# Kernel tuning notes

Measured on AMD Instinct MI355X. Metric: run time of the kernel, lower is better.

Reference implementation:

```python
import jax, jax.numpy as jnp
import numpy as np

N = 50000      # nodes
E = 1_600_000  # edges (avg degree 32)
IN, H, OUT, R = 128, 64, 32, 8
NEG_SLOPE = 0.2


def _rgat(x, src, dst, etype, W, q, k, b, n_nodes):
    """PyG RGATConv, defaults: heads=1, dim=1, additive-self-attention,
    across-relation softmax, concat=True, bias=True, dropout=0 (eval)."""
    # per-relation transform of all nodes: [R, N, O] (cheaper than per-edge bmm since 2*deg >> R)
    t = jnp.einsum('ni,rio->rno', x, W)
    xi = t[etype, dst]                      # [E, O] transformed target feats
    xj = t[etype, src]                      # [E, O] transformed source feats
    a = (xi @ q + xj @ k)[:, 0]             # [E] additive attention logits
    a = jnp.where(a >= 0, a, NEG_SLOPE * a)  # leaky_relu
    # segment softmax over incoming edges of each target node (across relations)
    m = jax.ops.segment_max(a, dst, num_segments=n_nodes)
    m = jnp.where(jnp.isfinite(m), m, 0.0)
    ex = jnp.exp(a - m[dst])
    s = jax.ops.segment_sum(ex, dst, num_segments=n_nodes)
    alpha = ex / (s[dst] + 1e-16)
    out = jax.ops.segment_sum(alpha[:, None] * xj, dst, num_segments=n_nodes)
    return out + b


def setup_inputs() -> dict:
    key = jax.random.key(0)
    ks = jax.random.split(key, 24)
    x = jax.random.normal(ks[0], (N, IN), jnp.float32)
    edge_index = jax.random.randint(ks[1], (2, E), 0, N, jnp.int32)
    edge_type = jax.random.randint(ks[2], (E,), 0, R, jnp.int32)

    def glorot(k, shape, fan_in):
        return jax.random.normal(k, shape, jnp.float32) * (1.0 / np.sqrt(fan_in))

    d = dict(x=x, edge_index=edge_index, edge_type=edge_type)
    # conv1: in->hidden, conv_mu / conv_logvar: hidden->hidden
    d['W1'] = glorot(ks[3], (R, IN, H), IN)
    d['q1'] = glorot(ks[4], (H, 1), H)
    d['k1'] = glorot(ks[5], (H, 1), H)
    d['b1'] = jnp.zeros((H,), jnp.float32)
    d['Wmu'] = glorot(ks[6], (R, H, H), H)
    d['qmu'] = glorot(ks[7], (H, 1), H)
    d['kmu'] = glorot(ks[8], (H, 1), H)
    d['bmu'] = jnp.zeros((H,), jnp.float32)
    d['Wlv'] = glorot(ks[9], (R, H, H), H)
    d['qlv'] = glorot(ks[10], (H, 1), H)
    d['klv'] = glorot(ks[11], (H, 1), H)
    d['blv'] = jnp.zeros((H,), jnp.float32)
    d['Wm'] = glorot(ks[12], (H, OUT), H)   # linear_mu (stored [in,out])
    d['bm'] = jnp.zeros((OUT,), jnp.float32)
    d['Wl'] = glorot(ks[13], (H, OUT), H)   # linear_logvar
    d['bl'] = jnp.zeros((OUT,), jnp.float32)
    return d


def reference(x, edge_index, edge_type, W1, q1, k1, b1,
              Wmu, qmu, kmu, bmu, Wlv, qlv, klv, blv, Wm, bm, Wl, bl):
    src, dst = edge_index[0], edge_index[1]
    hidden = jax.nn.relu(_rgat(x, src, dst, edge_type, W1, q1, k1, b1, N))
    mu = jax.nn.relu(_rgat(hidden, src, dst, edge_type, Wmu, qmu, kmu, bmu, N))
    mu = mu @ Wm + bm                       # dropout is identity in eval
    logvar = jax.nn.relu(_rgat(hidden, src, dst, edge_type, Wlv, qlv, klv, blv, N))
    logvar = logvar @ Wl + bl
    logstd = 0.5 * logvar
    return (mu, logstd)
```

## Files before the change

### kernel.cpp

```cpp
#include <hip/hip_runtime.h>
#include <cstdint>

#define HDIM 64
#define ODIM 32
#define NEG_SLOPE 0.2f
#define SCHUNK 2048
#define EPB 8192

typedef __attribute__((ext_vector_type(8))) short v8s;
typedef __attribute__((ext_vector_type(4))) float v4f;

__device__ __forceinline__ unsigned f2bf_rne(float f) {
  unsigned u = __float_as_uint(f);
  return (u + 0x7FFFu + ((u >> 16) & 1u)) >> 16;
}

__device__ __forceinline__ unsigned fenc(float f) {
  unsigned u = __float_as_uint(f);
  return (u & 0x80000000u) ? ~u : (u | 0x80000000u);
}
__device__ __forceinline__ float fdec(unsigned e) {
  unsigned u = (e & 0x80000000u) ? (e ^ 0x80000000u) : ~e;
  return __uint_as_float(u);
}

__global__ __launch_bounds__(256) void cvt_bf16_kernel(
    const float* __restrict__ in, unsigned short* __restrict__ out, int n) {
  int i = (blockIdx.x * 256 + threadIdx.x) * 4;
  if (i + 3 < n) {
    float4 v = *(const float4*)&in[i];
    ushort4 o;
    o.x = (unsigned short)f2bf_rne(v.x);
    o.y = (unsigned short)f2bf_rne(v.y);
    o.z = (unsigned short)f2bf_rne(v.z);
    o.w = (unsigned short)f2bf_rne(v.w);
    *(ushort4*)&out[i] = o;
  }
}

__global__ __launch_bounds__(256) void transpose_w_kernel(
    const float* __restrict__ W1, const float* __restrict__ Wmu,
    const float* __restrict__ Wlv, unsigned short* __restrict__ W1t,
    unsigned short* __restrict__ Wmut, unsigned short* __restrict__ Wlvt) {
  const int b = blockIdx.x;
  const int r = b & 7;
  const int which = b >> 3;
  const float* src;
  unsigned short* dst;
  int K;
  if (which == 0) {
    src = W1; dst = W1t; K = 128;
  } else if (which == 1) {
    src = Wmu; dst = Wmut; K = 64;
  } else {
    src = Wlv; dst = Wlvt; K = 64;
  }
  for (int idx = threadIdx.x; idx < K * 64; idx += 256) {
    const int kk = idx >> 6, o = idx & 63;
    dst[((size_t)r * 64 + o) * K + kk] =
        (unsigned short)f2bf_rne(src[((size_t)r * K + kk) * 64 + o]);
  }
}

__global__ __launch_bounds__(256) void count_deg_kernel(
    const int* __restrict__ dst, int* __restrict__ deg, int E) {
  int e = blockIdx.x * 256 + threadIdx.x;
  if (e < E) atomicAdd(&deg[dst[e]], 1);
}

__global__ __launch_bounds__(256) void scan_p1(const int* __restrict__ deg,
                                               int* __restrict__ bsum, int n) {
  int base = blockIdx.x * SCHUNK + threadIdx.x * 8;
  int s = 0;
#pragma unroll
  for (int j = 0; j < 8; j++) {
    int i = base + j;
    if (i < n) s += deg[i];
  }
#pragma unroll
  for (int d = 1; d < 64; d <<= 1) s += __shfl_xor(s, d, 64);
  __shared__ int ws[4];
  if ((threadIdx.x & 63) == 0) ws[threadIdx.x >> 6] = s;
  __syncthreads();
  if (threadIdx.x == 0) bsum[blockIdx.x] = ws[0] + ws[1] + ws[2] + ws[3];
}

__global__ void scan_p2(int* bsum, int nb) {
  int i = threadIdx.x;
  int v = (i < nb) ? bsum[i] : 0;
  int orig = v;
#pragma unroll
  for (int d = 1; d < 64; d <<= 1) {
    int up = __shfl_up(v, d, 64);
    if (i >= d) v += up;
  }
  if (i < nb) bsum[i] = v - orig;
}

__global__ __launch_bounds__(256) void scan_p3(const int* __restrict__ deg,
                                               const int* __restrict__ bsum,
                                               int* __restrict__ row_ptr,
                                               int n) {
  int base = blockIdx.x * SCHUNK + threadIdx.x * 8;
  int vals[8];
  int s = 0;
#pragma unroll
  for (int j = 0; j < 8; j++) {
    int i = base + j;
    vals[j] = (i < n) ? deg[i] : 0;
    s += vals[j];
  }
  int lane = threadIdx.x & 63, w = threadIdx.x >> 6;
  int v = s;
#pragma unroll
  for (int d = 1; d < 64; d <<= 1) {
    int up = __shfl_up(v, d, 64);
    if (lane >= d) v += up;
  }
  __shared__ int wsum[4];
  if (lane == 63) wsum[w] = v;
  __syncthreads();
  int woff = 0;
#pragma unroll
  for (int i = 0; i < 4; i++) woff += (i < w) ? wsum[i] : 0;
  int off = bsum[blockIdx.x] + woff + v - s;
#pragma unroll
  for (int j = 0; j < 8; j++) {
    int i = base + j;
    off += vals[j];
    if (i < n) row_ptr[i + 1] = off;
  }
  if (blockIdx.x == 0 && threadIdx.x == 0) row_ptr[0] = 0;
}

__global__ __launch_bounds__(256) void bucket_cursor_init(
    const int* __restrict__ row_ptr, int* __restrict__ cursor, int N, int nb) {
  int i = threadIdx.x;
  if (i < nb) cursor[i] = row_ptr[min(i * 256, N)];
}

__global__ __launch_bounds__(256) void bucket_pass1(
    const int* __restrict__ src, const int* __restrict__ dst,
    const int* __restrict__ etype, int* __restrict__ cursor,
    unsigned* __restrict__ tmp, int E) {
  __shared__ int hist[256];
  __shared__ int binstart[256];
  __shared__ int gbase[256];
  __shared__ int fill[256];
  __shared__ int wsum[4];
  __shared__ unsigned stage[EPB];
  __shared__ unsigned char binof[EPB];
  const int tid = threadIdx.x;
  const int e0 = blockIdx.x * EPB;
  const int cnt = min(EPB, E - e0);

  hist[tid] = 0;
  fill[tid] = 0;
  __syncthreads();
  for (int j = tid; j < cnt; j += 256) atomicAdd(&hist[dst[e0 + j] >> 8], 1);
  __syncthreads();

  const int hv = hist[tid];
  {
    const int lane = tid & 63, w = tid >> 6;
    int iv = hv;
#pragma unroll
    for (int d = 1; d < 64; d <<= 1) {
      int up = __shfl_up(iv, d, 64);
      if (lane >= d) iv += up;
    }
    if (lane == 63) wsum[w] = iv;
    __syncthreads();
    int woff = 0;
#pragma unroll
    for (int i = 0; i < 4; i++) woff += (i < w) ? wsum[i] : 0;
    binstart[tid] = woff + iv - hv;
    if (hv > 0) gbase[tid] = atomicAdd(&cursor[tid], hv);
  }
  __syncthreads();

  for (int j = tid; j < cnt; j += 256) {
    const int d = dst[e0 + j];
    const int b = d >> 8;
    const unsigned rec = ((unsigned)(d & 255) << 19) |
                         ((unsigned)etype[e0 + j] << 16) |
                         (unsigned)src[e0 + j];
    const int slot = binstart[b] + atomicAdd(&fill[b], 1);
    stage[slot] = rec;
    binof[slot] = (unsigned char)b;
  }
  __syncthreads();

  for (int s = tid; s < cnt; s += 256) {
    const int b = binof[s];
    tmp[gbase[b] + (s - binstart[b])] = stage[s];
  }
}

__global__ __launch_bounds__(256) void bucket_pass2(
    const int* __restrict__ row_ptr, const unsigned* __restrict__ tmp,
    int* __restrict__ edges, int N) {
  __shared__ int rp[257];
  __shared__ int fill[256];
  const int tid = threadIdx.x;
  const int rowbase = blockIdx.x * 256;
  const int rowcnt = min(256, N - rowbase);
  for (int i = tid; i <= rowcnt; i += 256) rp[i] = row_ptr[rowbase + i];
  fill[tid] = 0;
  __syncthreads();
  const int beg = rp[0];
  const int endv = rp[rowcnt];
  for (int i = beg + tid; i < endv; i += 256) {
    const unsigned rec = tmp[i];
    const int dlow = rec >> 19;
    const int pos = rp[dlow] + atomicAdd(&fill[dlow], 1);
    edges[pos] = (int)(rec & 0x7FFFFu);
  }
}

__global__ __launch_bounds__(256) void rowmax_kernel(
    const float* __restrict__ ak, unsigned* __restrict__ maxk_enc, int N) {
  const int row = blockIdx.x;
  const int nchunks = gridDim.y;
  const int per = (N + nchunks - 1) / nchunks;
  const int beg = blockIdx.y * per;
  const int end = min(N, beg + per);
  const float* r = ak + (size_t)row * N;
  float m = -1e30f;
  for (int i = beg + threadIdx.x; i < end; i += 256) m = fmaxf(m, r[i]);
#pragma unroll
  for (int d = 1; d < 64; d <<= 1) m = fmaxf(m, __shfl_xor(m, d, 64));
  __shared__ float ws[4];
  if ((threadIdx.x & 63) == 0) ws[threadIdx.x >> 6] = m;
  __syncthreads();
  if (threadIdx.x == 0) {
    float bm = fmaxf(fmaxf(ws[0], ws[1]), fmaxf(ws[2], ws[3]));
    atomicMax(&maxk_enc[row], fenc(bm));
  }
}

__global__ __launch_bounds__(256) void transform1_mfma(
    const unsigned short* __restrict__ xb,
    const unsigned short* __restrict__ W1t, const float* __restrict__ q,
    const float* __restrict__ k, unsigned short* __restrict__ tb,
    float* __restrict__ aq, float* __restrict__ ak, int N) {
  __shared__ unsigned short st[4][16][72];
  const int r = blockIdx.x;
  const int tid = threadIdx.x;
  const int w = tid >> 6;
  const int lane = tid & 63;
  const int quad = lane >> 4;
  const int mrow = lane & 15;
  const int n0w = blockIdx.y * 64 + w * 16;

  const int gA = min(n0w + mrow, N - 1);
  const unsigned short* arow = xb + (size_t)gA * 128 + quad * 8;
  const unsigned short* wrow = W1t + ((size_t)r * 64 + mrow) * 128 + quad * 8;

  v4f acc[4];
#pragma unroll
  for (int tt = 0; tt < 4; tt++) acc[tt] = (v4f){0.f, 0.f, 0.f, 0.f};

#pragma unroll
  for (int k0 = 0; k0 < 128; k0 += 32) {
    v8s a = *(const v8s*)(arow + k0);
#pragma unroll
    for (int tt = 0; tt < 4; tt++) {
      v8s b = *(const v8s*)(wrow + (size_t)tt * 16 * 128 + k0);
      acc[tt] = __builtin_amdgcn_mfma_f32_16x16x32_bf16(a, b, acc[tt], 0, 0, 0);
    }
  }

  float qv[4], kv[4];
#pragma unroll
  for (int tt = 0; tt < 4; tt++) {
    qv[tt] = q[tt * 16 + mrow];
    kv[tt] = k[tt * 16 + mrow];
  }

#pragma unroll
  for (int i = 0; i < 4; i++) {
    float vq = 0.f, vk = 0.f;
#pragma unroll
    for (int tt = 0; tt < 4; tt++) {
      vq = fmaf(acc[tt][i], qv[tt], vq);
      vk = fmaf(acc[tt][i], kv[tt], vk);
      st[w][quad * 4 + i][tt * 16 + mrow] =
          (unsigned short)f2bf_rne(acc[tt][i]);
    }
#pragma unroll
    for (int d = 1; d < 16; d <<= 1) {
      vq += __shfl_xor(vq, d, 64);
      vk += __shfl_xor(vk, d, 64);
    }
    const int gn = n0w + quad * 4 + i;
    if (mrow == 0 && gn < N) {
      aq[(size_t)r * N + gn] = vq;
      ak[(size_t)r * N + gn] = vk;
    }
  }
  __syncthreads();

  const int row = lane >> 2, cg = lane & 3;
  const int gns = n0w + row;
  if (gns < N) {
    const uint4 v0 = *(const uint4*)&st[w][row][cg * 16];
    const uint4 v1 = *(const uint4*)&st[w][row][cg * 16 + 8];
    uint4* dst = (uint4*)&tb[((size_t)r * N + gns) * 64 + cg * 16];
    dst[0] = v0;
    dst[1] = v1;
  }
}

__global__ __launch_bounds__(256) void transform2_mfma(
    const unsigned short* __restrict__ hb,
    const unsigned short* __restrict__ Wmut,
    const unsigned short* __restrict__ Wlvt, const float* __restrict__ qa,
    const float* __restrict__ ka, const float* __restrict__ qb,
    const float* __restrict__ kb, unsigned* __restrict__ t2p,
    float* __restrict__ aq2, float* __restrict__ ak2, int N) {
  __shared__ unsigned st2[4][16][68];
  const int r = blockIdx.x;
  const int tid = threadIdx.x;
  const int w = tid >> 6;
  const int lane = tid & 63;
  const int quad = lane >> 4;
  const int mrow = lane & 15;
  const int n0w = blockIdx.y * 64 + w * 16;

  const int gA = min(n0w + mrow, N - 1);
  const unsigned short* arow = hb + (size_t)gA * 64 + quad * 8;
  const size_t woff = ((size_t)r * 64 + mrow) * 64 + quad * 8;

  v4f am[4], al[4];
#pragma unroll
  for (int tt = 0; tt < 4; tt++) {
    am[tt] = (v4f){0.f, 0.f, 0.f, 0.f};
    al[tt] = (v4f){0.f, 0.f, 0.f, 0.f};
  }

#pragma unroll
  for (int k0 = 0; k0 < 64; k0 += 32) {
    v8s a = *(const v8s*)(arow + k0);
#pragma unroll
    for (int tt = 0; tt < 4; tt++) {
      v8s bm = *(const v8s*)(Wmut + woff + (size_t)tt * 16 * 64 + k0);
      v8s bl = *(const v8s*)(Wlvt + woff + (size_t)tt * 16 * 64 + k0);
      am[tt] = __builtin_amdgcn_mfma_f32_16x16x32_bf16(a, bm, am[tt], 0, 0, 0);
      al[tt] = __builtin_amdgcn_mfma_f32_16x16x32_bf16(a, bl, al[tt], 0, 0, 0);
    }
  }

  float qmv[4], kmv[4], qlv2[4], klv2[4];
#pragma unroll
  for (int tt = 0; tt < 4; tt++) {
    qmv[tt] = qa[tt * 16 + mrow];
    kmv[tt] = ka[tt * 16 + mrow];
    qlv2[tt] = qb[tt * 16 + mrow];
    klv2[tt] = kb[tt * 16 + mrow];
  }

#pragma unroll
  for (int i = 0; i < 4; i++) {
    float vqm = 0.f, vkm = 0.f, vql = 0.f, vkl = 0.f;
#pragma unroll
    for (int tt = 0; tt < 4; tt++) {
      vqm = fmaf(am[tt][i], qmv[tt], vqm);
      vkm = fmaf(am[tt][i], kmv[tt], vkm);
      vql = fmaf(al[tt][i], qlv2[tt], vql);
      vkl = fmaf(al[tt][i], klv2[tt], vkl);
      st2[w][quad * 4 + i][tt * 16 + mrow] =
          f2bf_rne(am[tt][i]) | (f2bf_rne(al[tt][i]) << 16);
    }
#pragma unroll
    for (int d = 1; d < 16; d <<= 1) {
      vqm += __shfl_xor(vqm, d, 64);
      vkm += __shfl_xor(vkm, d, 64);
      vql += __shfl_xor(vql, d, 64);
      vkl += __shfl_xor(vkl, d, 64);
    }
    const int gn = n0w + quad * 4 + i;
    if (mrow == 0 && gn < N) {
      aq2[(size_t)r * N + gn] = vqm;
      ak2[(size_t)r * N + gn] = vkm;
      aq2[(size_t)(8 + r) * N + gn] = vql;
      ak2[(size_t)(8 + r) * N + gn] = vkl;
    }
  }
  __syncthreads();

  const int row = lane >> 2, cg = lane & 3;
  const int gns = n0w + row;
  if (gns < N) {
    unsigned* dst = &t2p[((size_t)r * N + gns) * 64 + cg * 16];
#pragma unroll
    for (int s = 0; s < 4; s++)
      *(uint4*)(dst + s * 4) = *(const uint4*)&st2[w][row][cg * 16 + s * 4];
  }
}

__global__ __launch_bounds__(256) void aggregate_kernel(
    const int* __restrict__ row_ptr, const int* __restrict__ edges,
    const unsigned short* __restrict__ tb, const float* __restrict__ aq,
    const float* __restrict__ ak, const unsigned* __restrict__ maxk_enc,
    const float* __restrict__ bias, unsigned short* __restrict__ hb, int N) {
  const int tid = threadIdx.x;
  const int w = tid >> 6, o = tid & 63;
  int wid = blockIdx.x * 4 + w;
  const bool valid = wid < N;
  if (!valid) wid = N - 1;
  const int beg = row_ptr[wid];
  const int end = valid ? row_ptr[wid + 1] : beg;
  const int deg = end - beg;

  const float aqw = aq[(size_t)(o & 7) * N + wid];

  float v = aqw + fdec(maxk_enc[o & 7]);
  v = (v >= 0.f) ? v : NEG_SLOPE * v;
#pragma unroll
  for (int d = 1; d < 8; d <<= 1) v = fmaxf(v, __shfl_xor(v, d, 64));
  const float m = __shfl(v, 0, 64);

  float s = 0.f, acc = 0.f;
  for (int base = 0; base < deg; base += 64) {
    const int j = base + o;
    const int gcount = min(64, deg - base);
    const int packed = edges[beg + min(j, deg - 1)];
    const int src = packed & 0xFFFF;
    const int rr = packed >> 16;
    const int idx = rr * N + src;
    float x = __shfl(aqw, rr, 64) + ak[idx];
    x = (x >= 0.f) ? x : NEG_SLOPE * x;
    const float p = (j < deg) ? __expf(x - m) : 0.f;
    s += p;
    const int g8 = (gcount + 7) & ~7;
    for (int u = 0; u < g8; u += 8) {
      float pu[8];
      int iu[8];
#pragma unroll
      for (int q = 0; q < 8; q++) {
        pu[q] = __shfl(p, u + q, 64);
        iu[q] = __shfl(idx, u + q, 64);
      }
      unsigned short tv[8];
#pragma unroll
      for (int q = 0; q < 8; q++) tv[q] = tb[(size_t)iu[q] * 64 + o];
#pragma unroll
      for (int q = 0; q < 8; q++)
        acc = fmaf(pu[q], __uint_as_float((unsigned)tv[q] << 16), acc);
    }
  }
#pragma unroll
  for (int d = 1; d < 64; d <<= 1) s += __shfl_xor(s, d, 64);

  if (valid) {
    const float res = acc / (s + 1e-16f) + bias[o];
    hb[(size_t)wid * 64 + o] = (unsigned short)f2bf_rne(fmaxf(res, 0.f));
  }
}

__global__ __launch_bounds__(256) void aggregate2_kernel(
    const int* __restrict__ row_ptr, const int* __restrict__ edges,
    const unsigned* __restrict__ t2p, const float* __restrict__ aq2,
    const float* __restrict__ ak2, const unsigned* __restrict__ maxk2_enc,
    const float* __restrict__ bmu, const float* __restrict__ blv,
    const float* __restrict__ Wm, const float* __restrict__ bm,
    const float* __restrict__ Wlin, const float* __restrict__ bl,
    float* __restrict__ out_mu, float* __restrict__ out_ls, int N) {
  __shared__ float WmL[2048];
  __shared__ float WlL[2048];
  __shared__ float bL[64];
  __shared__ float hL[4][130];
  const int tid = threadIdx.x;
  for (int i = tid; i < 2048; i += 256) {
    WmL[i] = Wm[i];
    WlL[i] = Wlin[i];
  }
  if (tid < 32) {
    bL[tid] = bm[tid];
    bL[32 + tid] = bl[tid];
  }
  __syncthreads();

  const int w = tid >> 6, o = tid & 63;
  int wid = blockIdx.x * 4 + w;
  const bool valid = wid < N;
  if (!valid) wid = N - 1;
  const int beg = row_ptr[wid];
  const int end = valid ? row_ptr[wid + 1] : beg;
  const int deg = end - beg;

  const float aqw = aq2[(size_t)(o & 15) * N + wid];

  float v = aqw + fdec(maxk2_enc[o & 15]);
  v = (v >= 0.f) ? v : NEG_SLOPE * v;
#pragma unroll
  for (int d = 1; d < 8; d <<= 1) v = fmaxf(v, __shfl_xor(v, d, 64));
  const float m0 = __shfl(v, 0, 64);
  const float m1 = __shfl(v, 8, 64);

  float s0 = 0.f, s1 = 0.f, acc0 = 0.f, acc1 = 0.f;
  for (int base = 0; base < deg; base += 64) {
    const int j = base + o;
    const int gcount = min(64, deg - base);
    const int packed = edges[beg + min(j, deg - 1)];
    const int src = packed & 0xFFFF;
    const int rr = packed >> 16;
    const int idx = rr * N + src;
    float x0 = __shfl(aqw, rr, 64) + ak2[idx];
    float x1 = __shfl(aqw, 8 + rr, 64) + ak2[idx + 8 * N];
    x0 = (x0 >= 0.f) ? x0 : NEG_SLOPE * x0;
    x1 = (x1 >= 0.f) ? x1 : NEG_SLOPE * x1;
    const float p0 = (j < deg) ? __expf(x0 - m0) : 0.f;
    const float p1 = (j < deg) ? __expf(x1 - m1) : 0.f;
    s0 += p0;
    s1 += p1;
    const int g8 = (gcount + 7) & ~7;
    for (int u = 0; u < g8; u += 8) {
      float pu0[8], pu1[8];
      int iu[8];
#pragma unroll
      for (int q = 0; q < 8; q++) {
        pu0[q] = __shfl(p0, u + q, 64);
        pu1[q] = __shfl(p1, u + q, 64);
        iu[q] = __shfl(idx, u + q, 64);
      }
      unsigned pk[8];
#pragma unroll
      for (int q = 0; q < 8; q++) pk[q] = t2p[(size_t)iu[q] * 64 + o];
#pragma unroll
      for (int q = 0; q < 8; q++) {
        acc0 = fmaf(pu0[q], __uint_as_float(pk[q] << 16), acc0);
        acc1 = fmaf(pu1[q], __uint_as_float(pk[q] & 0xFFFF0000u), acc1);
      }
    }
  }
#pragma unroll
  for (int d = 1; d < 64; d <<= 1) {
    s0 += __shfl_xor(s0, d, 64);
    s1 += __shfl_xor(s1, d, 64);
  }

  const float h0 = fmaxf(acc0 / (s0 + 1e-16f) + bmu[o], 0.f);
  const float h1 = fmaxf(acc1 / (s1 + 1e-16f) + blv[o], 0.f);
  hL[w][o] = h0;
  hL[w][64 + o] = h1;
  __syncthreads();

  const float* hrow = &hL[w][(o >= 32) ? 64 : 0];
  const float* WL = (o >= 32) ? WlL : WmL;
  const int j = o & 31;
  float acc = 0.f;
#pragma unroll 8
  for (int c = 0; c < 64; c++) acc = fmaf(hrow[c], WL[c * 32 + j], acc);
  if (valid) {
    if (o < 32)
      out_mu[(size_t)wid * 32 + j] = acc + bL[j];
    else
      out_ls[(size_t)wid * 32 + j] = (acc + bL[32 + j]) * 0.5f;
  }
}

extern "C" void kernel_launch(void* const* d_in, const int* in_sizes, int n_in,
                              void* d_out, int out_size, void* d_ws,
                              size_t ws_size, hipStream_t stream) {
  const float* x = (const float*)d_in[0];
  const int* edge_index = (const int*)d_in[1];
  const int* edge_type = (const int*)d_in[2];
  const float* W1 = (const float*)d_in[3];
  const float* q1 = (const float*)d_in[4];
  const float* k1 = (const float*)d_in[5];
  const float* b1 = (const float*)d_in[6];
  const float* Wmu = (const float*)d_in[7];
  const float* qmu = (const float*)d_in[8];
  const float* kmu = (const float*)d_in[9];
  const float* bmu = (const float*)d_in[10];
  const float* Wlv = (const float*)d_in[11];
  const float* qlv = (const float*)d_in[12];
  const float* klv = (const float*)d_in[13];
  const float* blv = (const float*)d_in[14];
  const float* Wm = (const float*)d_in[15];
  const float* bm = (const float*)d_in[16];
  const float* Wl = (const float*)d_in[17];
  const float* bl = (const float*)d_in[18];

  const int N = in_sizes[0] / 128;
  const int E = in_sizes[2];
  const int R = in_sizes[3] / (128 * 64);

  float* out_mu = (float*)d_out;
  float* out_ls = (float*)d_out + (size_t)N * ODIM;

  char* wsp = (char*)d_ws;
  size_t off = 0;
  auto carve = [&](size_t bytes) {
    void* p = wsp + off;
    off += (bytes + 255) & ~(size_t)255;
    return p;
  };

  void* tbuf = carve((size_t)R * N * 64 * sizeof(unsigned));
  unsigned short* t1b = (unsigned short*)tbuf;
  unsigned* t2p = (unsigned*)tbuf;
  unsigned short* xb = (unsigned short*)carve((size_t)N * 128 * 2);
  unsigned short* hb = (unsigned short*)carve((size_t)N * 64 * 2);
  unsigned short* W1t = (unsigned short*)carve((size_t)R * 64 * 128 * 2);
  unsigned short* Wmut = (unsigned short*)carve((size_t)R * 64 * 64 * 2);
  unsigned short* Wlvt = (unsigned short*)carve((size_t)R * 64 * 64 * 2);
  float* aq2 = (float*)carve((size_t)2 * R * N * sizeof(float));
  float* ak2 = (float*)carve((size_t)2 * R * N * sizeof(float));
  unsigned* maxk_enc = (unsigned*)carve(2 * R * sizeof(unsigned));
  int* deg = (int*)carve((size_t)N * sizeof(int));
  int* row_ptr = (int*)carve((size_t)(N + 1) * sizeof(int));
  int* bsum = (int*)carve(256 * sizeof(int));
  int* cursor = (int*)carve(256 * sizeof(int));
  unsigned* tmp = (unsigned*)carve((size_t)E * sizeof(unsigned));
  int* edges = (int*)carve((size_t)E * sizeof(int));

  const int* e_src = edge_index;
  const int* e_dst = edge_index + E;

  cvt_bf16_kernel<<<(N * 128 / 4 + 255) / 256, 256, 0, stream>>>(x, xb,
                                                                 N * 128);
  transpose_w_kernel<<<3 * R, 256, 0, stream>>>(W1, Wmu, Wlv, W1t, Wmut, Wlvt);

  hipMemsetAsync(deg, 0, (size_t)N * sizeof(int), stream);
  hipMemsetAsync(maxk_enc, 0, 2 * R * sizeof(unsigned), stream);
  count_deg_kernel<<<(E + 255) / 256, 256, 0, stream>>>(e_dst, deg, E);
  const int nchunk = (N + SCHUNK - 1) / SCHUNK;
  scan_p1<<<nchunk, 256, 0, stream>>>(deg, bsum, N);
  scan_p2<<<1, 64, 0, stream>>>(bsum, nchunk);
  scan_p3<<<nchunk, 256, 0, stream>>>(deg, bsum, row_ptr, N);

  const int nbuck = (N + 255) >> 8;
  bucket_cursor_init<<<1, 256, 0, stream>>>(row_ptr, cursor, N, nbuck);
  bucket_pass1<<<(E + EPB - 1) / EPB, 256, 0, stream>>>(e_src, e_dst,
                                                        edge_type, cursor,
                                                        tmp, E);
  bucket_pass2<<<nbuck, 256, 0, stream>>>(row_ptr, tmp, edges, N);

  const int nb64 = (N + 63) / 64;
  const int agg_blocks = (N + 3) / 4;

  transform1_mfma<<<dim3(R, nb64), 256, 0, stream>>>(xb, W1t, q1, k1, t1b,
                                                     aq2, ak2, N);
  rowmax_kernel<<<dim3(R, 32), 256, 0, stream>>>(ak2, maxk_enc, N);
  aggregate_kernel<<<agg_blocks, 256, 0, stream>>>(
      row_ptr, edges, t1b, aq2, ak2, maxk_enc, b1, hb, N);

  hipMemsetAsync(maxk_enc, 0, 2 * R * sizeof(unsigned), stream);

  transform2_mfma<<<dim3(R, nb64), 256, 0, stream>>>(
      hb, Wmut, Wlvt, qmu, kmu, qlv, klv, t2p, aq2, ak2, N);
  rowmax_kernel<<<dim3(2 * R, 32), 256, 0, stream>>>(ak2, maxk_enc, N);
  aggregate2_kernel<<<agg_blocks, 256, 0, stream>>>(
      row_ptr, edges, t2p, aq2, ak2, maxk_enc, bmu, blv, Wm, bm, Wl, bl,
      out_mu, out_ls, N);
}
```

Baseline: 562.4 us.

## Vectorize neighbor feature gathers with 16-byte loads across edge-parallel lane groups

Both aggregation kernels now split each wavefront into lane groups that each handle a different edge. Each lane loads a 16-byte chunk of the neighbor's bf16 feature row and keeps several per-channel accumulators, which are summed across groups with xor-shuffles at the end. Previously every lane issued a 2- or 4-byte gather per edge, so this cuts the number of memory instructions and shuffles per edge. In exchange it adds a cross-lane reduction, more registers and padding waste when degree is not a multiple of the group count.

```diff
diff --git a/kernel.cpp b/kernel.cpp
--- a/kernel.cpp
+++ b/kernel.cpp
@@ -421,7 +421,13 @@
   for (int d = 1; d < 8; d <<= 1) v = fmaxf(v, __shfl_xor(v, d, 64));
   const float m = __shfl(v, 0, 64);
 
-  float s = 0.f, acc = 0.f;
+  const int g = o >> 3;
+  const int cl = o & 7;
+  float s = 0.f;
+  float acc[8];
+#pragma unroll
+  for (int c = 0; c < 8; c++) acc[c] = 0.f;
+
   for (int base = 0; base < deg; base += 64) {
     const int j = base + o;
     const int gcount = min(64, deg - base);
@@ -434,28 +440,45 @@
     const float p = (j < deg) ? __expf(x - m) : 0.f;
     s += p;
     const int g8 = (gcount + 7) & ~7;
+#pragma unroll 4
     for (int u = 0; u < g8; u += 8) {
-      float pu[8];
-      int iu[8];
-#pragma unroll
-      for (int q = 0; q < 8; q++) {
-        pu[q] = __shfl(p, u + q, 64);
-        iu[q] = __shfl(idx, u + q, 64);
-      }
-      unsigned short tv[8];
-#pragma unroll
-      for (int q = 0; q < 8; q++) tv[q] = tb[(size_t)iu[q] * 64 + o];
-#pragma unroll
-      for (int q = 0; q < 8; q++)
-        acc = fmaf(pu[q], __uint_as_float((unsigned)tv[q] << 16), acc);
+      const int e = u + g;
+      const float pe = __shfl(p, e, 64);
+      const int ie = __shfl(idx, e, 64);
+      const uint4 tv = *(const uint4*)(tb + (size_t)ie * 64 + cl * 8);
+      const unsigned uu0 = tv.x, uu1 = tv.y, uu2 = tv.z, uu3 = tv.w;
+      acc[0] = fmaf(pe, __uint_as_float(uu0 << 16), acc[0]);
+      acc[1] = fmaf(pe, __uint_as_float(uu0 & 0xFFFF0000u), acc[1]);
+      acc[2] = fmaf(pe, __uint_as_float(uu1 << 16), acc[2]);
+      acc[3] = fmaf(pe, __uint_as_float(uu1 & 0xFFFF0000u), acc[3]);
+      acc[4] = fmaf(pe, __uint_as_float(uu2 << 16), acc[4]);
+      acc[5] = fmaf(pe, __uint_as_float(uu2 & 0xFFFF0000u), acc[5]);
+      acc[6] = fmaf(pe, __uint_as_float(uu3 << 16), acc[6]);
+      acc[7] = fmaf(pe, __uint_as_float(uu3 & 0xFFFF0000u), acc[7]);
     }
   }
 #pragma unroll
   for (int d = 1; d < 64; d <<= 1) s += __shfl_xor(s, d, 64);
-
-  if (valid) {
-    const float res = acc / (s + 1e-16f) + bias[o];
-    hb[(size_t)wid * 64 + o] = (unsigned short)f2bf_rne(fmaxf(res, 0.f));
+#pragma unroll
+  for (int d = 8; d < 64; d <<= 1) {
+#pragma unroll
+    for (int c = 0; c < 8; c++) acc[c] += __shfl_xor(acc[c], d, 64);
+  }
+
+  if (valid && g == 0) {
+    const float inv = 1.f / (s + 1e-16f);
+    unsigned rv[8];
+#pragma unroll
+    for (int c = 0; c < 8; c++) {
+      const float res = acc[c] * inv + bias[cl * 8 + c];
+      rv[c] = f2bf_rne(fmaxf(res, 0.f));
+    }
+    uint4 pkd;
+    pkd.x = rv[0] | (rv[1] << 16);
+    pkd.y = rv[2] | (rv[3] << 16);
+    pkd.z = rv[4] | (rv[5] << 16);
+    pkd.w = rv[6] | (rv[7] << 16);
+    *(uint4*)(hb + (size_t)wid * 64 + cl * 8) = pkd;
   }
 }
 
@@ -499,7 +522,16 @@
   const float m0 = __shfl(v, 0, 64);
   const float m1 = __shfl(v, 8, 64);
 
-  float s0 = 0.f, s1 = 0.f, acc0 = 0.f, acc1 = 0.f;
+  const int g = o >> 4;
+  const int cl = o & 15;
+  float s0 = 0.f, s1 = 0.f;
+  float acc0[4], acc1[4];
+#pragma unroll
+  for (int c = 0; c < 4; c++) {
+    acc0[c] = 0.f;
+    acc1[c] = 0.f;
+  }
+
   for (int base = 0; base < deg; base += 64) {
     const int j = base + o;
     const int gcount = min(64, deg - base);
@@ -515,24 +547,23 @@
     const float p1 = (j < deg) ? __expf(x1 - m1) : 0.f;
     s0 += p0;
     s1 += p1;
-    const int g8 = (gcount + 7) & ~7;
-    for (int u = 0; u < g8; u += 8) {
-      float pu0[8], pu1[8];
-      int iu[8];
-#pragma unroll
-      for (int q = 0; q < 8; q++) {
-        pu0[q] = __shfl(p0, u + q, 64);
-        pu1[q] = __shfl(p1, u + q, 64);
-        iu[q] = __shfl(idx, u + q, 64);
-      }
-      unsigned pk[8];
-#pragma unroll
-      for (int q = 0; q < 8; q++) pk[q] = t2p[(size_t)iu[q] * 64 + o];
-#pragma unroll
-      for (int q = 0; q < 8; q++) {
-        acc0 = fmaf(pu0[q], __uint_as_float(pk[q] << 16), acc0);
-        acc1 = fmaf(pu1[q], __uint_as_float(pk[q] & 0xFFFF0000u), acc1);
-      }
+    const int g4 = (gcount + 3) & ~3;
+#pragma unroll 4
+    for (int u = 0; u < g4; u += 4) {
+      const int e = u + g;
+      const float pe0 = __shfl(p0, e, 64);
+      const float pe1 = __shfl(p1, e, 64);
+      const int ie = __shfl(idx, e, 64);
+      const uint4 pk = *(const uint4*)(t2p + (size_t)ie * 64 + cl * 4);
+      const unsigned uu0 = pk.x, uu1 = pk.y, uu2 = pk.z, uu3 = pk.w;
+      acc0[0] = fmaf(pe0, __uint_as_float(uu0 << 16), acc0[0]);
+      acc1[0] = fmaf(pe1, __uint_as_float(uu0 & 0xFFFF0000u), acc1[0]);
+      acc0[1] = fmaf(pe0, __uint_as_float(uu1 << 16), acc0[1]);
+      acc1[1] = fmaf(pe1, __uint_as_float(uu1 & 0xFFFF0000u), acc1[1]);
+      acc0[2] = fmaf(pe0, __uint_as_float(uu2 << 16), acc0[2]);
+      acc1[2] = fmaf(pe1, __uint_as_float(uu2 & 0xFFFF0000u), acc1[2]);
+      acc0[3] = fmaf(pe0, __uint_as_float(uu3 << 16), acc0[3]);
+      acc1[3] = fmaf(pe1, __uint_as_float(uu3 & 0xFFFF0000u), acc1[3]);
     }
   }
 #pragma unroll
@@ -540,11 +571,24 @@
     s0 += __shfl_xor(s0, d, 64);
     s1 += __shfl_xor(s1, d, 64);
   }
-
-  const float h0 = fmaxf(acc0 / (s0 + 1e-16f) + bmu[o], 0.f);
-  const float h1 = fmaxf(acc1 / (s1 + 1e-16f) + blv[o], 0.f);
-  hL[w][o] = h0;
-  hL[w][64 + o] = h1;
+#pragma unroll
+  for (int d = 16; d < 64; d <<= 1) {
+#pragma unroll
+    for (int c = 0; c < 4; c++) {
+      acc0[c] += __shfl_xor(acc0[c], d, 64);
+      acc1[c] += __shfl_xor(acc1[c], d, 64);
+    }
+  }
+
+  if (g == 0) {
+    const float inv0 = 1.f / (s0 + 1e-16f);
+    const float inv1 = 1.f / (s1 + 1e-16f);
+#pragma unroll
+    for (int c = 0; c < 4; c++) {
+      hL[w][cl * 4 + c] = fmaxf(acc0[c] * inv0 + bmu[cl * 4 + c], 0.f);
+      hL[w][64 + cl * 4 + c] = fmaxf(acc1[c] * inv1 + blv[cl * 4 + c], 0.f);
+    }
+  }
   __syncthreads();
 
   const float* hrow = &hL[w][(o >= 32) ? 64 : 0];
```

Result: no change. 554.6 us (-1.4%).
